# Kernel optimization log

Measured on AMD Instinct MI355X. Metric: run time of the kernel, lower is better.

Reference implementation:

```python
import jax, jax.numpy as jnp
import numpy as np

B, T, D, H, L, V = 2, 1024, 768, 12, 8, 32000
HD = D // H


def setup_inputs() -> dict:
    key = jax.random.key(0)
    ks = jax.random.split(key, 16)
    init = lambda k, shape: jax.random.normal(k, shape, jnp.float32) * 0.02
    return {
        "idx": jax.random.randint(ks[0], (B, T), 0, V),
        "targets": jax.random.randint(ks[1], (B, T), 0, V),
        "tok_emb": init(ks[2], (V, D)),
        "pos_emb": init(ks[3], (T, D)),
        "ln1_w": jnp.ones((L, D)), "ln1_b": jnp.zeros((L, D)),
        "wq": init(ks[4], (L, D, D)),  # per-head D->HD projections stacked columnwise
        "wk": init(ks[5], (L, D, D)),
        "wv": init(ks[6], (L, D, D)),
        "wo": init(ks[7], (L, D, D)), "bo": jnp.zeros((L, D)),
        "ln2_w": jnp.ones((L, D)), "ln2_b": jnp.zeros((L, D)),
        "w1": init(ks[8], (L, D, 4 * D)), "b1": jnp.zeros((L, 4 * D)),
        "w2": init(ks[9], (L, 4 * D, D)), "b2": jnp.zeros((L, D)),
        "lnf_w": jnp.ones((D,)), "lnf_b": jnp.zeros((D,)),
        "lm_w": init(ks[10], (D, V)), "lm_b": jnp.zeros((V,)),
    }


def _ln(x, w, b):
    m = x.mean(-1, keepdims=True)
    v = x.var(-1, keepdims=True)
    return (x - m) * jax.lax.rsqrt(v + 1e-5) * w + b


def _gpt(idx, targets, tok_emb, pos_emb, ln1_w, ln1_b, wq, wk, wv, wo, bo,
         ln2_w, ln2_b, w1, b1, w2, b2, lnf_w, lnf_b, lm_w, lm_b):
    x = tok_emb[idx] + pos_emb[None, :T]          # [B,T,D]
    mask = jnp.tril(jnp.ones((T, T), bool))
    scale = D ** -0.5  # NOTE: original scales by embedding_dim**-0.5 (C), not head_size

    def block(x, p):
        l1w, l1b, Wq, Wk, Wv, Wo, Bo, l2w, l2b, W1, B1, W2, B2 = p
        h = _ln(x, l1w, l1b)
        q = (h @ Wq).reshape(B, T, H, HD)
        k = (h @ Wk).reshape(B, T, H, HD)
        v = (h @ Wv).reshape(B, T, H, HD)
        s = jnp.einsum('bqhd,bkhd->bhqk', q, k) * scale
        s = jnp.where(mask, s, -jnp.inf)
        a = jax.nn.softmax(s, axis=-1)
        o = jnp.einsum('bhqk,bkhd->bqhd', a, v).reshape(B, T, D)
        x = x + o @ Wo + Bo
        h = _ln(x, l2w, l2b)
        x = x + jax.nn.gelu(h @ W1 + B1, approximate=False) @ W2 + B2
        return x, None

    x, _ = jax.lax.scan(block, x, (ln1_w, ln1_b, wq, wk, wv, wo, bo,
                                   ln2_w, ln2_b, w1, b1, w2, b2))
    x = _ln(x, lnf_w, lnf_b)
    logits = (x @ lm_w + lm_b).reshape(B * T, V)
    logp = jax.nn.log_softmax(logits, axis=-1)
    loss = -jnp.take_along_axis(logp, targets.reshape(-1, 1), axis=1).mean()
    return logits, loss


def reference(idx, targets, tok_emb, pos_emb, ln1_w, ln1_b, wq, wk, wv, wo, bo,
              ln2_w, ln2_b, w1, b1, w2, b2, lnf_w, lnf_b, lm_w, lm_b):
    return _gpt(idx, targets, tok_emb, pos_emb, ln1_w, ln1_b, wq, wk, wv, wo, bo,
                ln2_w, ln2_b, w1, b1, w2, b2, lnf_w, lnf_b, lm_w, lm_b)
```

## Files before the change

kernel.cpp:

```cpp
#include <hip/hip_runtime.h>

#define Bz   2
#define Tz   1024
#define Dz   768
#define Hz   12
#define HDz  64
#define Lz   8
#define Vz   32000
#define BTz  (Bz*Tz)
#define DFz  (4*Dz)
#define PLWz 7077888L
#define NPART 500
#define SCALEz 0.036084391824351615f

typedef __attribute__((ext_vector_type(4))) short s16x4;
typedef __attribute__((ext_vector_type(8))) short s16x8;
typedef __attribute__((ext_vector_type(4))) float f32x4;

__device__ __forceinline__ short f2b(float f) {
    union { float f; unsigned u; } v; v.f = f;
    unsigned r = v.u + 0x7fffu + ((v.u >> 16) & 1u);
    return (short)(r >> 16);
}

__device__ __forceinline__ void gload16(const short* g, short* l) {
    __builtin_amdgcn_global_load_lds(
        (const __attribute__((address_space(1))) void*)g,
        (__attribute__((address_space(3))) void*)l, 16, 0, 0);
}

#define MFMA32(a,b,c) __builtin_amdgcn_mfma_f32_16x16x32_bf16(a,b,c,0,0,0)

__global__ __launch_bounds__(256)
void tconv_k(const float* __restrict__ in, short* __restrict__ out,
             int K, int N, int ldin)
{
    __shared__ float tl[32][33];
    const int tx = threadIdx.x & 31, ty = threadIdx.x >> 5;
    const int n0 = blockIdx.x * 32, k0 = blockIdx.y * 32;
    #pragma unroll
    for (int i = 0; i < 4; i++)
        tl[ty + i*8][tx] = in[(long)(k0 + ty + i*8)*ldin + n0 + tx];
    __syncthreads();
    #pragma unroll
    for (int i = 0; i < 4; i++)
        out[(long)(n0 + ty + i*8)*K + k0 + tx] = f2b(tl[tx][ty + i*8]);
}

__global__ __launch_bounds__(256)
void wconv_all(const float* __restrict__ wq, const float* __restrict__ wk,
               const float* __restrict__ wv, const float* __restrict__ wo,
               const float* __restrict__ w1, const float* __restrict__ w2,
               short* __restrict__ wall, int l0)
{
    const int l = l0 + blockIdx.y;
    short* dst = wall + (long)blockIdx.y * PLWz;
    int t = blockIdx.x;
    const float* src; long doff; int K, N, ldin, nx;
    if (t < 2304) {
        int m = t / 576; t -= m * 576;
        src = (m==0 ? wq : m==1 ? wk : m==2 ? wv : wo) + (long)l * 589824;
        doff = (long)m * 589824; K = 768; N = 768; ldin = 768; nx = 24;
    } else if (t < 4608) {
        t -= 2304;
        src = w1 + (long)l * 2359296; doff = 2359296; K = 768; N = 3072; ldin = 3072; nx = 96;
    } else {
        t -= 4608;
        src = w2 + (long)l * 2359296; doff = 4718592; K = 3072; N = 768; ldin = 768; nx = 24;
    }
    const int n0 = (t % nx) * 32, k0 = (t / nx) * 32;
    __shared__ float tl[32][33];
    const int tx = threadIdx.x & 31, ty = threadIdx.x >> 5;
    #pragma unroll
    for (int i = 0; i < 4; i++)
        tl[ty + i*8][tx] = src[(long)(k0 + ty + i*8)*ldin + n0 + tx];
    __syncthreads();
    short* o = dst + doff;
    #pragma unroll
    for (int i = 0; i < 4; i++)
        o[(long)(n0 + ty + i*8)*K + k0 + tx] = f2b(tl[tx][ty + i*8]);
}

template<int BM, int EPI, bool OUTBF, bool MRAST = false, bool LOSSP = false>
__global__ __launch_bounds__(256)
void gemm2(const short* __restrict__ A, const short* __restrict__ Bt,
           const float* __restrict__ bias, const float* __restrict__ resp,
           void* __restrict__ Cv, int K, int ldc, float2* __restrict__ part)
{
    constexpr int BN = 128, BK = 64;
    constexpr int WTM = BM/2;
    constexpr int AM = WTM/16;
    __shared__ short Al[BM*BK];
    __shared__ short Bl[BN*BK];
    const int bx = MRAST ? blockIdx.y : blockIdx.x;
    const int by = MRAST ? blockIdx.x : blockIdx.y;
    const int m0 = by*BM, n0 = bx*BN;
    const int tid = threadIdx.x, lane = tid & 63, wid = tid >> 6;
    const int wm = wid >> 1, wn = wid & 1;
    const int r = lane & 15, kg = lane >> 4;
    const int arow = lane >> 3, acol = (lane & 7)*8;

    const short* ga = A  + (long)(m0 + wid*(BM/4) + arow)*K + acol;
    const short* gb = Bt + (long)(n0 + wid*32     + arow)*K + acol;
    short* la = &Al[(wid*(BM/4))*BK];
    short* lb = &Bl[(wid*32)*BK];

    f32x4 acc[AM][4] = {};

    for (int k0 = 0; k0 < K; k0 += BK) {
        #pragma unroll
        for (int i = 0; i < BM/32; i++)
            gload16(ga + (long)i*8*K + k0, la + i*8*BK);
        #pragma unroll
        for (int i = 0; i < 4; i++)
            gload16(gb + (long)i*8*K + k0, lb + i*8*BK);
        __syncthreads();
        #pragma unroll
        for (int ks = 0; ks < 2; ks++) {
            s16x8 af[AM], bf[4];
            #pragma unroll
            for (int mI = 0; mI < AM; mI++)
                af[mI] = *(const s16x8*)&Al[(wm*WTM + mI*16 + r)*BK + ks*32 + kg*8];
            #pragma unroll
            for (int nI = 0; nI < 4; nI++)
                bf[nI] = *(const s16x8*)&Bl[(wn*64 + nI*16 + r)*BK + ks*32 + kg*8];
            #pragma unroll
            for (int mI = 0; mI < AM; mI++)
                #pragma unroll
                for (int nI = 0; nI < 4; nI++)
                    acc[mI][nI] = MFMA32(af[mI], bf[nI], acc[mI][nI]);
        }
        __syncthreads();
    }

    float bnv[4] = {0.f, 0.f, 0.f, 0.f};
    if constexpr (EPI >= 1) {
        #pragma unroll
        for (int nI = 0; nI < 4; nI++) bnv[nI] = bias[n0 + wn*64 + nI*16 + r];
    }

    #pragma unroll
    for (int mI = 0; mI < AM; mI++) {
        #pragma unroll
        for (int nI = 0; nI < 4; nI++) {
            #pragma unroll
            for (int reg = 0; reg < 4; reg++) {
                int row = wm*WTM + mI*16 + kg*4 + reg;
                int col = wn*64 + nI*16 + r;
                long off = (long)(m0+row)*ldc + (n0+col);
                float v = acc[mI][nI][reg] + bnv[nI];
                if constexpr (EPI == 2) v += resp[off];
                if constexpr (EPI == 3) v = 0.5f*v*(1.0f + erff(v*0.70710678118654752f));
                if constexpr (OUTBF) ((short*)Cv)[off] = f2b(v);
                else                 ((float*)Cv)[off] = v;
            }
        }
    }

    if constexpr (LOSSP) {
        #pragma unroll
        for (int mI = 0; mI < AM; mI++) {
            #pragma unroll
            for (int reg = 0; reg < 4; reg++) {
                float mx = -3.4e38f;
                #pragma unroll
                for (int nI = 0; nI < 4; nI++)
                    mx = fmaxf(mx, acc[mI][nI][reg] + bnv[nI]);
                #pragma unroll
                for (int o = 1; o < 16; o <<= 1)
                    mx = fmaxf(mx, __shfl_xor(mx, o));
                float s = 0.f;
                #pragma unroll
                for (int nI = 0; nI < 4; nI++)
                    s += __expf(acc[mI][nI][reg] + bnv[nI] - mx);
                #pragma unroll
                for (int o = 1; o < 16; o <<= 1)
                    s += __shfl_xor(s, o);
                if (r == 0) {
                    int row = m0 + wm*WTM + mI*16 + kg*4 + reg;
                    part[(long)row*NPART + bx*2 + wn] = make_float2(mx, s);
                }
            }
        }
    }
}

__global__ __launch_bounds__(256)
void attn_k(const short* __restrict__ qkv, short* __restrict__ att)
{
    const int w = threadIdx.x >> 6;
    const int lane = threadIdx.x & 63;
    const int r = lane & 15, kg = lane >> 4;
    const int hd0 = blockIdx.y * HDz;
    const long brow = (long)blockIdx.z * Tz;
    const int q0w = blockIdx.x * 64 + w * 16;
    const int qi = q0w + r;

    const short* qp = qkv + (brow + q0w + r) * 2304 + hd0;
    const s16x8 qf0 = *(const s16x8*)(qp + kg*8);
    const s16x8 qf1 = *(const s16x8*)(qp + 32 + kg*8);
    const short* kb = qkv + brow * 2304 + 768 + hd0;
    const short* vb = qkv + brow * 2304 + 1536 + hd0;

    float m = -3.4e38f, l = 0.f;
    f32x4 ot[4] = {};

    const int ntiles = blockIdx.x * 4 + w + 1;
    for (int t = 0; t < ntiles; t++) {
        const int kt = t * 16;
        const short* kp = kb + (long)(kt + r) * 2304;
        s16x8 kf0 = *(const s16x8*)(kp + kg*8);
        s16x8 kf1 = *(const s16x8*)(kp + 32 + kg*8);
        f32x4 z = {};
        f32x4 st = MFMA32(kf0, qf0, z);
        st = MFMA32(kf1, qf1, st);
        float s4[4];
        #pragma unroll
        for (int j = 0; j < 4; j++) {
            int ki = kt + kg*4 + j;
            s4[j] = (ki <= qi) ? st[j]*SCALEz : -1e30f;
        }
        float cm = fmaxf(fmaxf(s4[0], s4[1]), fmaxf(s4[2], s4[3]));
        cm = fmaxf(cm, __shfl_xor(cm, 16));
        cm = fmaxf(cm, __shfl_xor(cm, 32));
        float mn = fmaxf(m, cm);
        float alpha = __expf(m - mn);
        float p0 = __expf(s4[0]-mn), p1 = __expf(s4[1]-mn);
        float p2 = __expf(s4[2]-mn), p3 = __expf(s4[3]-mn);
        l = l*alpha + (p0+p1+p2+p3);
        m = mn;
        s16x8 pb = { f2b(p0), f2b(p1), f2b(p2), f2b(p3), 0, 0, 0, 0 };
        #pragma unroll
        for (int d0 = 0; d0 < 4; d0++) {
            const short* vp = vb + (long)(kt + kg*4)*2304 + d0*16 + r;
            s16x8 va = { vp[0], vp[2304], vp[4608], vp[6912], 0, 0, 0, 0 };
            f32x4 o = ot[d0];
            o[0]*=alpha; o[1]*=alpha; o[2]*=alpha; o[3]*=alpha;
            ot[d0] = MFMA32(va, pb, o);
        }
    }
    l += __shfl_xor(l, 16);
    l += __shfl_xor(l, 32);
    const float inv = 1.f / l;
    short* ap = att + (brow + q0w + r)*Dz + hd0;
    #pragma unroll
    for (int d0 = 0; d0 < 4; d0++) {
        s16x4 pk = { f2b(ot[d0][0]*inv), f2b(ot[d0][1]*inv),
                     f2b(ot[d0][2]*inv), f2b(ot[d0][3]*inv) };
        *(s16x4*)(ap + d0*16 + kg*4) = pk;
    }
}

__global__ void embed_k(const int* __restrict__ idx, const float* __restrict__ tok,
                        const float* __restrict__ pos, float* __restrict__ x)
{
    int qi = blockIdx.x*blockDim.x + threadIdx.x;
    if (qi >= BTz*(Dz/4)) return;
    int row = qi / (Dz/4);
    int c   = (qi % (Dz/4)) * 4;
    int token = idx[row];
    int tpos  = row & (Tz-1);
    float4 a = *reinterpret_cast<const float4*>(tok + (long)token*Dz + c);
    float4 p = *reinterpret_cast<const float4*>(pos + (long)tpos*Dz + c);
    float4 o; o.x=a.x+p.x; o.y=a.y+p.y; o.z=a.z+p.z; o.w=a.w+p.w;
    *reinterpret_cast<float4*>(x + (long)row*Dz + c) = o;
}

__global__ __launch_bounds__(256)
void ln_k(const float* __restrict__ x, const float* __restrict__ w,
          const float* __restrict__ b, short* __restrict__ y)
{
    const int lane = threadIdx.x & 63;
    const int row = blockIdx.x*4 + (threadIdx.x >> 6);
    const float* xr = x + (long)row*Dz;
    float4 v[3];
    #pragma unroll
    for (int j = 0; j < 3; j++) v[j] = *(const float4*)(xr + lane*4 + j*256);
    float s = 0.f, ss = 0.f;
    #pragma unroll
    for (int j = 0; j < 3; j++) {
        s  += v[j].x + v[j].y + v[j].z + v[j].w;
        ss += v[j].x*v[j].x + v[j].y*v[j].y + v[j].z*v[j].z + v[j].w*v[j].w;
    }
    #pragma unroll
    for (int o = 32; o > 0; o >>= 1) {
        s += __shfl_xor(s, o); ss += __shfl_xor(ss, o);
    }
    float mean = s * (1.0f/Dz);
    float var  = ss * (1.0f/Dz) - mean*mean;
    float rs = rsqrtf(var + 1e-5f);
    short* yr = y + (long)row*Dz;
    #pragma unroll
    for (int j = 0; j < 3; j++) {
        float4 wj = *(const float4*)(w + lane*4 + j*256);
        float4 bj = *(const float4*)(b + lane*4 + j*256);
        s16x4 pk = { f2b((v[j].x-mean)*rs*wj.x + bj.x),
                     f2b((v[j].y-mean)*rs*wj.y + bj.y),
                     f2b((v[j].z-mean)*rs*wj.z + bj.z),
                     f2b((v[j].w-mean)*rs*wj.w + bj.w) };
        *(s16x4*)(yr + lane*4 + j*256) = pk;
    }
}

__global__ __launch_bounds__(256)
void lossfin_k(const float* __restrict__ logits, const float2* __restrict__ part,
               const int* __restrict__ tgt, float* __restrict__ row_loss)
{
    const int row = blockIdx.x, t = threadIdx.x;
    float m = -3.4e38f, s = 0.f;
    for (int i = t; i < NPART; i += 256) {
        float2 p = part[(long)row*NPART + i];
        float M = fmaxf(m, p.x);
        s = s*__expf(m - M) + p.y*__expf(p.x - M);
        m = M;
    }
    __shared__ float smm[256], sms[256];
    smm[t] = m; sms[t] = s; __syncthreads();
    for (int k = 128; k > 0; k >>= 1) {
        if (t < k) {
            float M = fmaxf(smm[t], smm[t+k]);
            sms[t] = sms[t]*__expf(smm[t]-M) + sms[t+k]*__expf(smm[t+k]-M);
            smm[t] = M;
        }
        __syncthreads();
    }
    if (t == 0)
        row_loss[row] = smm[0] + logf(sms[0]) - logits[(long)row*Vz + tgt[row]];
}

__global__ __launch_bounds__(256)
void loss_rows_k(const float* __restrict__ logits, const int* __restrict__ tgt,
                 float* __restrict__ row_loss)
{
    int row = blockIdx.x;
    const float* lr = logits + (long)row*Vz;
    const float4* lr4 = (const float4*)lr;
    int t = threadIdx.x;
    __shared__ float sm[256];
    float mx = -3.4e38f;
    for (int c = t; c < Vz/4; c += 256) {
        float4 f = lr4[c];
        mx = fmaxf(mx, fmaxf(fmaxf(f.x, f.y), fmaxf(f.z, f.w)));
    }
    sm[t] = mx; __syncthreads();
    for (int k = 128; k > 0; k >>= 1) { if (t < k) sm[t] = fmaxf(sm[t], sm[t+k]); __syncthreads(); }
    float m = sm[0]; __syncthreads();
    float s = 0.f;
    for (int c = t; c < Vz/4; c += 256) {
        float4 f = lr4[c];
        s += expf(f.x-m) + expf(f.y-m) + expf(f.z-m) + expf(f.w-m);
    }
    sm[t] = s; __syncthreads();
    for (int k = 128; k > 0; k >>= 1) { if (t < k) sm[t] += sm[t+k]; __syncthreads(); }
    if (t == 0) {
        float logZ = m + logf(sm[0]);
        row_loss[row] = logZ - lr[tgt[row]];
    }
}

__global__ void loss_reduce_k(const float* __restrict__ row_loss, float* __restrict__ out)
{
    __shared__ float sm[256];
    int t = threadIdx.x;
    float s = 0.f;
    for (int i = t; i < BTz; i += 256) s += row_loss[i];
    sm[t] = s; __syncthreads();
    for (int k = 128; k > 0; k >>= 1) { if (t < k) sm[t] += sm[t+k]; __syncthreads(); }
    if (t == 0) out[0] = sm[0] * (1.0f/BTz);
}

extern "C" void kernel_launch(void* const* d_in, const int* in_sizes, int n_in,
                              void* d_out, int out_size, void* d_ws, size_t ws_size,
                              hipStream_t stream)
{
    const int*   idx     = (const int*)  d_in[0];
    const int*   tgt     = (const int*)  d_in[1];
    const float* tok_emb = (const float*)d_in[2];
    const float* pos_emb = (const float*)d_in[3];
    const float* ln1_w   = (const float*)d_in[4];
    const float* ln1_b   = (const float*)d_in[5];
    const float* wq      = (const float*)d_in[6];
    const float* wk      = (const float*)d_in[7];
    const float* wv      = (const float*)d_in[8];
    const float* wo      = (const float*)d_in[9];
    const float* bo      = (const float*)d_in[10];
    const float* ln2_w   = (const float*)d_in[11];
    const float* ln2_b   = (const float*)d_in[12];
    const float* w1      = (const float*)d_in[13];
    const float* b1      = (const float*)d_in[14];
    const float* w2      = (const float*)d_in[15];
    const float* b2      = (const float*)d_in[16];
    const float* lnf_w   = (const float*)d_in[17];
    const float* lnf_b   = (const float*)d_in[18];
    const float* lm_w    = (const float*)d_in[19];
    const float* lm_b    = (const float*)d_in[20];

    float* logits = (float*)d_out;
    float* loss   = logits + (long)BTz*Vz;

    char* p = (char*)d_ws;
    float*  x     = (float*)p;  p += (long)BTz*Dz*4;
    float*  rloss = (float*)p;  p += BTz*4;
    float2* part  = (float2*)p; p += (long)BTz*NPART*8;
    short*  h     = (short*)p;  p += (long)BTz*Dz*2;
    short*  qkvb  = (short*)p;  p += (long)BTz*2304*2;
    short*  attb  = (short*)p;  p += (long)BTz*Dz*2;
    short*  midb  = (short*)p;  p += (long)BTz*DFz*2;
    short*  wall  = (short*)p;
    size_t fixed = (size_t)(p - (char*)d_ws);
    const long LMT = (long)Vz*Dz;
    bool upfront = ws_size >= fixed + (size_t)(8*PLWz + LMT)*2;
    short* lmt = wall + (upfront ? 8*PLWz : PLWz);

    embed_k<<<dim3((BTz*(Dz/4) + 255)/256), 256, 0, stream>>>(idx, tok_emb, pos_emb, x);

    if (upfront) {
        wconv_all<<<dim3(6912, 8), 256, 0, stream>>>(wq, wk, wv, wo, w1, w2, wall, 0);
        tconv_k<<<dim3(Vz/32, 24), 256, 0, stream>>>(lm_w, lmt, Dz, Vz, Vz);
    }

    for (int l = 0; l < Lz; l++) {
        short* wl = wall + (upfront ? (long)l*PLWz : 0);
        if (!upfront)
            wconv_all<<<dim3(6912, 1), 256, 0, stream>>>(wq, wk, wv, wo, w1, w2, wall, l);

        ln_k<<<BTz/4, 256, 0, stream>>>(x, ln1_w + l*Dz, ln1_b + l*Dz, h);
        gemm2<128,0,true><<<dim3(18,16), 256, 0, stream>>>(
            h, wl, nullptr, nullptr, qkvb, Dz, 2304, nullptr);
        attn_k<<<dim3(Tz/64, Hz, Bz), 256, 0, stream>>>(qkvb, attb);
        gemm2<64,2,false><<<dim3(6,32), 256, 0, stream>>>(
            attb, wl + 1769472, bo + l*Dz, x, x, Dz, Dz, nullptr);
        ln_k<<<BTz/4, 256, 0, stream>>>(x, ln2_w + l*Dz, ln2_b + l*Dz, h);
        gemm2<128,3,true><<<dim3(24,16), 256, 0, stream>>>(
            h, wl + 2359296, b1 + l*DFz, nullptr, midb, Dz, DFz, nullptr);
        gemm2<64,2,false><<<dim3(6,32), 256, 0, stream>>>(
            midb, wl + 4718592, b2 + l*Dz, x, x, DFz, Dz, nullptr);
    }

    ln_k<<<BTz/4, 256, 0, stream>>>(x, lnf_w, lnf_b, h);
    if (upfront) {
        gemm2<128,1,false,true,true><<<dim3(16, Vz/128), 256, 0, stream>>>(
            h, lmt, lm_b, nullptr, logits, Dz, Vz, part);
        lossfin_k<<<BTz, 256, 0, stream>>>(logits, part, tgt, rloss);
    } else {
        for (int c = 0; c < Vz; c += 8192) {
            int cn = (Vz - c < 8192) ? (Vz - c) : 8192;
            tconv_k<<<dim3(cn/32, 24), 256, 0, stream>>>(lm_w + c, lmt, Dz, cn, Vz);
            gemm2<128,1,false><<<dim3(cn/128, 16), 256, 0, stream>>>(
                h, lmt, lm_b + c, nullptr, logits + c, Dz, Vz, nullptr);
        }
        loss_rows_k<<<BTz, 256, 0, stream>>>(logits, tgt, rloss);
    }
    loss_reduce_k<<<1, 256, 0, stream>>>(rloss, loss);
}
```

Before: 1.809 ms.

## Double-buffer GEMM LDS tiles and swizzle LM-head block order

Gives the bf16 GEMM two LDS buffers so global loads for the next K tile are issued before the MFMAs on the current tile, leaving one barrier per iteration instead of two. The LM-head GEMM also switches from M-major rasterisation to a grouped swizzle, where each group of 8 N-column blocks covers all 16 M blocks, to improve L2 reuse of the weight tiles. Extra blocks past the vocabulary return early. The change doubles LDS use per block, which may lower occupancy, and overlap depends on the async load path.

```diff
diff --git a/kernel.cpp b/kernel.cpp
--- a/kernel.cpp
+++ b/kernel.cpp
@@ -81,7 +81,7 @@
         o[(long)(n0 + ty + i*8)*K + k0 + tx] = f2b(tl[tx][ty + i*8]);
 }
 
-template<int BM, int EPI, bool OUTBF, bool MRAST = false, bool LOSSP = false>
+template<int BM, int EPI, bool OUTBF, bool SWZ = false, bool LOSSP = false>
 __global__ __launch_bounds__(256)
 void gemm2(const short* __restrict__ A, const short* __restrict__ Bt,
            const float* __restrict__ bias, const float* __restrict__ resp,
@@ -90,10 +90,15 @@
     constexpr int BN = 128, BK = 64;
     constexpr int WTM = BM/2;
     constexpr int AM = WTM/16;
-    __shared__ short Al[BM*BK];
-    __shared__ short Bl[BN*BK];
-    const int bx = MRAST ? blockIdx.y : blockIdx.x;
-    const int by = MRAST ? blockIdx.x : blockIdx.y;
+    __shared__ short Al[2][BM*BK];
+    __shared__ short Bl[2][BN*BK];
+    int bx, by;
+    if constexpr (SWZ) {
+        const int sub = blockIdx.x;
+        bx = blockIdx.y*8 + (sub & 7);
+        by = sub >> 3;
+        if (bx >= Vz/BN) return;
+    } else { bx = blockIdx.x; by = blockIdx.y; }
     const int m0 = by*BM, n0 = bx*BN;
     const int tid = threadIdx.x, lane = tid & 63, wid = tid >> 6;
     const int wm = wid >> 1, wn = wid & 1;
@@ -102,28 +107,37 @@
 
     const short* ga = A  + (long)(m0 + wid*(BM/4) + arow)*K + acol;
     const short* gb = Bt + (long)(n0 + wid*32     + arow)*K + acol;
-    short* la = &Al[(wid*(BM/4))*BK];
-    short* lb = &Bl[(wid*32)*BK];
-
-    f32x4 acc[AM][4] = {};
-
-    for (int k0 = 0; k0 < K; k0 += BK) {
+    const int laoff = (wid*(BM/4))*BK;
+    const int lboff = (wid*32)*BK;
+
+    auto stage = [&](int buf, int k0) {
+        short* la = &Al[buf][laoff];
+        short* lb = &Bl[buf][lboff];
         #pragma unroll
         for (int i = 0; i < BM/32; i++)
             gload16(ga + (long)i*8*K + k0, la + i*8*BK);
         #pragma unroll
         for (int i = 0; i < 4; i++)
             gload16(gb + (long)i*8*K + k0, lb + i*8*BK);
-        __syncthreads();
+    };
+
+    f32x4 acc[AM][4] = {};
+    const int nk = K / BK;
+
+    stage(0, 0);
+    __syncthreads();
+    int cur = 0;
+    for (int t = 0; t < nk; t++) {
+        if (t + 1 < nk) stage(cur ^ 1, (t + 1)*BK);
         #pragma unroll
         for (int ks = 0; ks < 2; ks++) {
             s16x8 af[AM], bf[4];
             #pragma unroll
             for (int mI = 0; mI < AM; mI++)
-                af[mI] = *(const s16x8*)&Al[(wm*WTM + mI*16 + r)*BK + ks*32 + kg*8];
+                af[mI] = *(const s16x8*)&Al[cur][(wm*WTM + mI*16 + r)*BK + ks*32 + kg*8];
             #pragma unroll
             for (int nI = 0; nI < 4; nI++)
-                bf[nI] = *(const s16x8*)&Bl[(wn*64 + nI*16 + r)*BK + ks*32 + kg*8];
+                bf[nI] = *(const s16x8*)&Bl[cur][(wn*64 + nI*16 + r)*BK + ks*32 + kg*8];
             #pragma unroll
             for (int mI = 0; mI < AM; mI++)
                 #pragma unroll
@@ -131,6 +145,7 @@
                     acc[mI][nI] = MFMA32(af[mI], bf[nI], acc[mI][nI]);
         }
         __syncthreads();
+        cur ^= 1;
     }
 
     float bnv[4] = {0.f, 0.f, 0.f, 0.f};
@@ -439,7 +454,7 @@
 
     ln_k<<<BTz/4, 256, 0, stream>>>(x, lnf_w, lnf_b, h);
     if (upfront) {
-        gemm2<128,1,false,true,true><<<dim3(16, Vz/128), 256, 0, stream>>>(
+        gemm2<128,1,false,true,true><<<dim3(128, 32), 256, 0, stream>>>(
             h, lmt, lm_b, nullptr, logits, Dz, Vz, part);
         lossfin_k<<<BTz, 256, 0, stream>>>(logits, part, tgt, rloss);
     } else {
```

New measurement: 1.799 ms. No clear change (-0.5%).
